# Kernel optimization log

Hardware: AMD Instinct MI355X
Metric: run time of the kernel (lower is better)

## Reference

```python
import jax, jax.numpy as jnp
import numpy as np

B, L, D, H = 4, 2048, 1024, 16
HD = D // H

def setup_inputs() -> dict:
    key = jax.random.key(0)
    k1, k2, k3, k4 = jax.random.split(key, 4)
    return {
        "Q": jax.random.normal(k1, (B, L, D), dtype=jnp.float32),
        "K": jax.random.normal(k2, (B, L, D), dtype=jnp.float32),
        "V": jax.random.normal(k3, (B, L, D), dtype=jnp.float32),
        "W_out": jax.random.normal(k4, (D, D), dtype=jnp.float32) * (1.0 / np.sqrt(D)),
        "b_out": jnp.zeros((D,), dtype=jnp.float32),
    }

def reference(Q, K, V, W_out, b_out):
    b, l, d = Q.shape
    h, hd = H, d // H
    q = Q.reshape(b, l, h, hd)
    k = K.reshape(b, l, h, hd)
    v = V.reshape(b, l, h, hd)
    # energy: [b, h, q, k]
    energy = jnp.einsum('nqhd,nkhd->nhqk', q, k)
    # NOTE: original scales by sqrt(embed_dim), not sqrt(head_dim)
    attn = jax.nn.softmax(energy / jnp.sqrt(jnp.float32(d)), axis=-1)
    out = jnp.einsum('nhql,nlhd->nqhd', attn, v).reshape(b, l, d)
    # torch nn.Linear: x @ W.T + b
    return out @ W_out.T + b_out
```

## Files before the change

### kernel.cpp

```cpp
#include <hip/hip_runtime.h>
#include <hip/hip_bf16.h>


#define B_  4
#define L_  2048
#define D_  1024
#define H_  16

typedef float  f32x4  __attribute__((ext_vector_type(4)));
typedef float  f32x16 __attribute__((ext_vector_type(16)));
typedef short  bf16x8 __attribute__((ext_vector_type(8)));
typedef short  bf16x4 __attribute__((ext_vector_type(4)));

__device__ inline unsigned short f2bf(float x) {
    union { float f; unsigned u; } v; v.f = x;
    unsigned r = v.u + 0x7FFFu + ((v.u >> 16) & 1u);
    return (unsigned short)(r >> 16);
}
__device__ inline float fast_exp2(float x) {
#if __has_builtin(__builtin_amdgcn_exp2f)
    return __builtin_amdgcn_exp2f(x);
#else
    return exp2f(x);
#endif
}
__device__ inline bf16x8 pack8s(float4 a, float4 b, float s) {
    bf16x8 r;
    r[0] = (short)f2bf(a.x * s); r[1] = (short)f2bf(a.y * s);
    r[2] = (short)f2bf(a.z * s); r[3] = (short)f2bf(a.w * s);
    r[4] = (short)f2bf(b.x * s); r[5] = (short)f2bf(b.y * s);
    r[6] = (short)f2bf(b.z * s); r[7] = (short)f2bf(b.w * s);
    return r;
}
__device__ inline unsigned cvtpk(float lo, float hi) {
    unsigned r;
    asm("v_cvt_pk_bf16_f32 %0, %1, %2" : "=v"(r) : "v"(lo), "v"(hi));
    return r;
}
#define PSWAP(a, b) asm("v_permlane32_swap_b32 %0, %1" : "+v"(a), "+v"(b))

__device__ inline f32x16 zero16() {
    f32x16 z;
    #pragma unroll
    for (int i = 0; i < 16; ++i) z[i] = 0.f;
    return z;
}
__device__ inline void gld16(const void* g, void* l) {
    __builtin_amdgcn_global_load_lds(
        (const __attribute__((address_space(1))) void*)g,
        (__attribute__((address_space(3))) void*)l, 16, 0, 0);
}

__global__ __launch_bounds__(256) void convw_kernel(const float* __restrict__ W,
                                                    unsigned short* __restrict__ Wb) {
    int i = (blockIdx.x * 256 + threadIdx.x) * 4;
    float4 v = *(const float4*)&W[i];
    bf16x4 o;
    o[0] = (short)f2bf(v.x); o[1] = (short)f2bf(v.y);
    o[2] = (short)f2bf(v.z); o[3] = (short)f2bf(v.w);
    *(bf16x4*)&Wb[i] = o;
}

__global__ __launch_bounds__(256) void convk_kernel(const float* __restrict__ K,
                                                    unsigned short* __restrict__ Kb) {
    int o = blockIdx.x * 256 + threadIdx.x;
    int d8 = o & 7; int h = (o >> 3) & 15; int key = (o >> 7) & 2047; int b = o >> 18;
    size_t base = ((size_t)(b * L_ + key) * H_ + h) * 64;
    const float* p = K + base + d8 * 8;
    float4 a = *(const float4*)p, c = *(const float4*)(p + 4);
    bf16x8 r;
    r[0] = (short)f2bf(a.x); r[1] = (short)f2bf(a.y); r[2] = (short)f2bf(a.z); r[3] = (short)f2bf(a.w);
    r[4] = (short)f2bf(c.x); r[5] = (short)f2bf(c.y); r[6] = (short)f2bf(c.z); r[7] = (short)f2bf(c.w);
    *(bf16x8*)&Kb[base + ((d8 * 8) ^ ((key & 7) * 8))] = r;
}

__global__ __launch_bounds__(256) void convv_kernel(const float* __restrict__ V,
                                                    unsigned short* __restrict__ Vb) {
    __shared__ __align__(16) unsigned short T[64 * 72];
    int tid = threadIdx.x;
    int kb_ = blockIdx.x & 31, bh = blockIdx.x >> 5;
    int b = bh >> 4, h = bh & 15, k0 = kb_ * 64;
    int kl = tid >> 4;
    int d4 = (tid & 15) * 4;
    #pragma unroll
    for (int pp = 0; pp < 4; ++pp) {
        int key = pp * 16 + kl;
        const float* p = V + ((size_t)(b * L_ + k0 + key)) * D_ + h * 64 + d4;
        float4 v = *(const float4*)p;
        T[(d4 + 0) * 72 + key] = f2bf(v.x);
        T[(d4 + 1) * 72 + key] = f2bf(v.y);
        T[(d4 + 2) * 72 + key] = f2bf(v.z);
        T[(d4 + 3) * 72 + key] = f2bf(v.w);
    }
    __syncthreads();
    #pragma unroll
    for (int i = 0; i < 2; ++i) {
        int c = i * 256 + tid; int d = c >> 3, ch = c & 7;
        bf16x8 v = *(const bf16x8*)&T[d * 72 + ch * 8];
        *(bf16x8*)&Vb[((size_t)(b * H_ + h) * 64 + d) * L_ + k0 + ((ch ^ (d & 7)) * 8)] = v;
    }
}

__global__ __launch_bounds__(256, 4) void attn_kernel(const float* __restrict__ Qg,
                                                      const unsigned short* __restrict__ Kb,
                                                      const unsigned short* __restrict__ Vb,
                                                      unsigned short* __restrict__ Og) {
    __shared__ __align__(16) unsigned short Ks[2][64 * 64];
    __shared__ __align__(16) unsigned short Vt[2][64 * 64];

    const int tid  = threadIdx.x;
    const int w    = tid >> 6;
    const int lane = tid & 63;
    const int l31  = lane & 31;
    const int hl   = lane >> 5;
    const int r7   = l31 & 7;

    const int x   = blockIdx.x;
    const int idx = x >> 3;
    const int bh  = (x & 7) * 8 + (idx & 7);
    const int qb  = idx >> 3;
    const int bz  = bh >> 4;
    const int h   = bh & 15;
    const int q0  = qb * 128;

    const float qscale = 0.04508422f;
    bf16x8 bq[4];
    {
        const int qrow = q0 + w * 32 + l31;
        const float* qp = Qg + ((size_t)(bz * L_ + qrow)) * D_ + h * 64 + hl * 8;
        #pragma unroll
        for (int dstep = 0; dstep < 4; ++dstep)
            bq[dstep] = pack8s(*(const float4*)(qp + dstep * 16),
                               *(const float4*)(qp + dstep * 16 + 4), qscale);
    }

    f32x16 o[2];
    o[0] = zero16(); o[1] = zero16();
    float lsum = 0.f;

    const unsigned short* Kbh = Kb + ((size_t)bz * L_ * H_ + h) * 64;
    const unsigned short* Vbh = Vb + (size_t)(bz * H_ + h) * 64 * L_;

    #define ISSUE(T, BUF)                                                           \
        {                                                                           \
            int k0_ = (T) * 64;                                                     \
            _Pragma("unroll")                                                       \
            for (int i = 0; i < 2; ++i) {                                           \
                int c = i * 256 + tid; int rr = c >> 3, jj = c & 7;                 \
                gld16(Kbh + (size_t)(k0_ + rr) * (H_ * 64) + jj * 8,                \
                      (char*)Ks[BUF] + (i * 256 + w * 64) * 16);                    \
                gld16(Vbh + (size_t)rr * L_ + k0_ + jj * 8,                         \
                      (char*)Vt[BUF] + (i * 256 + w * 64) * 16);                    \
            }                                                                       \
        }

    ISSUE(0, 0)

    for (int t = 0; t < 32; ++t) {
        __syncthreads();
        if (t < 31) ISSUE(t + 1, (t + 1) & 1)
        const unsigned short* ks = Ks[t & 1];
        const unsigned short* vt = Vt[t & 1];

        #pragma unroll
        for (int kk = 0; kk < 2; ++kk) {
            f32x16 s = zero16();
            #pragma unroll
            for (int dstep = 0; dstep < 4; ++dstep) {
                bf16x8 kf = *(const bf16x8*)&ks[(kk * 32 + l31) * 64 +
                                                ((((dstep << 1) | hl) ^ r7) << 3)];
                s = __builtin_amdgcn_mfma_f32_32x32x16_bf16(kf, bq[dstep], s, 0, 0, 0);
            }

            float p_[16];
            #pragma unroll
            for (int r = 0; r < 16; ++r) p_[r] = fast_exp2(s[r]);
            lsum += ((p_[0] + p_[1]) + (p_[2] + p_[3])) + ((p_[4] + p_[5]) + (p_[6] + p_[7]))
                  + ((p_[8] + p_[9]) + (p_[10] + p_[11])) + ((p_[12] + p_[13]) + (p_[14] + p_[15]));
            unsigned pk_[8];
            #pragma unroll
            for (int j = 0; j < 8; ++j) pk_[j] = cvtpk(p_[2 * j], p_[2 * j + 1]);
            PSWAP(pk_[0], pk_[2]); PSWAP(pk_[1], pk_[3]);
            PSWAP(pk_[4], pk_[6]); PSWAP(pk_[5], pk_[7]);
            union { unsigned u[4]; bf16x8 v; } a0_, a1_;
            a0_.u[0] = pk_[0]; a0_.u[1] = pk_[1]; a0_.u[2] = pk_[2]; a0_.u[3] = pk_[3];
            a1_.u[0] = pk_[4]; a1_.u[1] = pk_[5]; a1_.u[2] = pk_[6]; a1_.u[3] = pk_[7];

            #pragma unroll
            for (int kh = 0; kh < 2; ++kh) {
                const bf16x8 pf = kh ? a1_.v : a0_.v;
                const int kk2 = kk * 2 + kh;
                bf16x8 v0 = *(const bf16x8*)&vt[(l31) * 64 +
                                                ((((kk2 << 1) | hl) ^ r7) << 3)];
                bf16x8 v1 = *(const bf16x8*)&vt[(32 + l31) * 64 +
                                                ((((kk2 << 1) | hl) ^ r7) << 3)];
                o[0] = __builtin_amdgcn_mfma_f32_32x32x16_bf16(pf, v0, o[0], 0, 0, 0);
                o[1] = __builtin_amdgcn_mfma_f32_32x32x16_bf16(pf, v1, o[1], 0, 0, 0);
            }
        }
    }

    float tot = lsum + __shfl_xor(lsum, 32);
    float inv = 1.0f / tot;
    const size_t rowb0 = ((size_t)(bz * L_ + q0 + w * 32)) * D_ + h * 64;
    #pragma unroll
    for (int r = 0; r < 16; ++r) {
        const int qloc = (r & 3) + 8 * (r >> 2) + 4 * hl;
        const float invr = __shfl(inv, qloc);
        unsigned short* op = Og + rowb0 + (size_t)qloc * D_;
        op[l31]      = f2bf(o[0][r] * invr);
        op[32 + l31] = f2bf(o[1][r] * invr);
    }
}

__global__ __launch_bounds__(256, 2) void proj_kernel(const unsigned short* __restrict__ Og,
                                                      const unsigned short* __restrict__ Wb,
                                                      const float* __restrict__ bias,
                                                      float* __restrict__ Yg) {
    __shared__ unsigned short As[2][128 * 64];
    __shared__ unsigned short Bs[2][128 * 64];

    const int tid  = threadIdx.x;
    const int w    = tid >> 6;
    const int lane = tid & 63;
    const int l16  = lane & 15;
    const int quad = lane >> 4;
    const int wm   = w & 1, wn = w >> 1;

    const int m0 = blockIdx.x * 128;
    const int n0 = blockIdx.y * 128;

    f32x4 acc[4][4];
    #pragma unroll
    for (int i = 0; i < 4; ++i)
        #pragma unroll
        for (int j = 0; j < 4; ++j) acc[i][j] = (f32x4){0.f, 0.f, 0.f, 0.f};

    #define PISSUE(T, BUF)                                                          \
        {                                                                           \
            int kt_ = (T) * 64;                                                     \
            _Pragma("unroll")                                                       \
            for (int i = 0; i < 4; ++i) {                                           \
                int c = i * 256 + tid; int row = c >> 3, p = c & 7;                 \
                int j = p ^ (row & 7);                                              \
                gld16(&Og[(size_t)(m0 + row) * 1024 + kt_ + j * 8],                 \
                      (char*)As[BUF] + (i * 256 + w * 64) * 16);                    \
                gld16(&Wb[(size_t)(n0 + row) * 1024 + kt_ + j * 8],                 \
                      (char*)Bs[BUF] + (i * 256 + w * 64) * 16);                    \
            }                                                                       \
        }

    PISSUE(0, 0)

    for (int t = 0; t < 16; ++t) {
        __syncthreads();
        if (t < 15) PISSUE(t + 1, (t + 1) & 1)
        const unsigned short* as = As[t & 1];
        const unsigned short* bs = Bs[t & 1];

        #pragma unroll
        for (int ksq = 0; ksq < 2; ++ksq) {
            bf16x8 a[4], b[4];
            #pragma unroll
            for (int mt = 0; mt < 4; ++mt) {
                int row = wm * 64 + mt * 16 + l16;
                a[mt] = *(const bf16x8*)&as[row * 64 + (((ksq * 4 + quad) ^ (l16 & 7)) * 8)];
            }
            #pragma unroll
            for (int nt = 0; nt < 4; ++nt) {
                int row = wn * 64 + nt * 16 + l16;
                b[nt] = *(const bf16x8*)&bs[row * 64 + (((ksq * 4 + quad) ^ (l16 & 7)) * 8)];
            }
            #pragma unroll
            for (int mt = 0; mt < 4; ++mt)
                #pragma unroll
                for (int nt = 0; nt < 4; ++nt)
                    acc[mt][nt] = __builtin_amdgcn_mfma_f32_16x16x32_bf16(a[mt], b[nt], acc[mt][nt], 0, 0, 0);
        }
    }

    #pragma unroll
    for (int mt = 0; mt < 4; ++mt)
        #pragma unroll
        for (int nt = 0; nt < 4; ++nt) {
            int e = n0 + wn * 64 + nt * 16 + l16;
            float bv = bias[e];
            #pragma unroll
            for (int r = 0; r < 4; ++r) {
                int m = m0 + wm * 64 + mt * 16 + quad * 4 + r;
                Yg[(size_t)m * 1024 + e] = acc[mt][nt][r] + bv;
            }
        }
}

extern "C" void kernel_launch(void* const* d_in, const int* in_sizes, int n_in,
                              void* d_out, int out_size, void* d_ws, size_t ws_size,
                              hipStream_t stream) {
    const float* Q    = (const float*)d_in[0];
    const float* K    = (const float*)d_in[1];
    const float* V    = (const float*)d_in[2];
    const float* W    = (const float*)d_in[3];
    const float* bias = (const float*)d_in[4];
    float* Y = (float*)d_out;

    unsigned short* Og = (unsigned short*)d_ws;
    unsigned short* Wb = (unsigned short*)((char*)d_ws + (size_t)16 * 1024 * 1024);
    unsigned short* Kb = (unsigned short*)d_out;
    unsigned short* Vb = Kb + (size_t)B_ * H_ * L_ * 64;

    convw_kernel<<<D_ * D_ / (256 * 4), 256, 0, stream>>>(W, Wb);
    convk_kernel<<<B_ * L_ * H_ * 8 / 256, 256, 0, stream>>>(K, Kb);
    convv_kernel<<<B_ * H_ * (L_ / 64), 256, 0, stream>>>(V, Vb);
    attn_kernel<<<B_ * H_ * (L_ / 128), 256, 0, stream>>>(Q, Kb, Vb, Og);
    dim3 pg(B_ * L_ / 128, D_ / 128);
    proj_kernel<<<pg, 256, 0, stream>>>(Og, Wb, bias, Y);
}
```

Baseline: 237.6 us.

## Use 128-key tiles, MFMA row sums, and setprio in attention loop

The attention kernel now processes 128 keys per pipeline stage instead of 64. This halves the number of barrier and prefetch iterations, and it doubles the shared memory per block, so launch bounds drop from 4 to 2 blocks per CU. The softmax denominator is now computed with an extra MFMA against a vector of ones, replacing the scalar adds and the final cross-lane shuffle. That adds two MFMAs per subtile and sums the bf16-rounded probabilities, which slightly changes the numerics. s_setprio hints are also wrapped around the MFMA sections to favour matrix issue.

```diff
diff --git a/kernel.cpp b/kernel.cpp
--- a/kernel.cpp
+++ b/kernel.cpp
@@ -101,12 +101,12 @@
     }
 }
 
-__global__ __launch_bounds__(256, 4) void attn_kernel(const float* __restrict__ Qg,
+__global__ __launch_bounds__(256, 2) void attn_kernel(const float* __restrict__ Qg,
                                                       const unsigned short* __restrict__ Kb,
                                                       const unsigned short* __restrict__ Vb,
                                                       unsigned short* __restrict__ Og) {
-    __shared__ __align__(16) unsigned short Ks[2][64 * 64];
-    __shared__ __align__(16) unsigned short Vt[2][64 * 64];
+    __shared__ __align__(16) unsigned short Ks[2][128 * 64];
+    __shared__ __align__(16) unsigned short Vt[2][64 * 128];
 
     const int tid  = threadIdx.x;
     const int w    = tid >> 6;
@@ -134,49 +134,55 @@
                                *(const float4*)(qp + dstep * 16 + 4), qscale);
     }
 
+    bf16x8 ones;
+    #pragma unroll
+    for (int j = 0; j < 8; ++j) ones[j] = (short)0x3F80;
+
     f32x16 o[2];
     o[0] = zero16(); o[1] = zero16();
-    float lsum = 0.f;
+    f32x16 sums = zero16();
 
     const unsigned short* Kbh = Kb + ((size_t)bz * L_ * H_ + h) * 64;
     const unsigned short* Vbh = Vb + (size_t)(bz * H_ + h) * 64 * L_;
 
     #define ISSUE(T, BUF)                                                           \
         {                                                                           \
-            int k0_ = (T) * 64;                                                     \
+            int k0_ = (T) * 128;                                                    \
             _Pragma("unroll")                                                       \
-            for (int i = 0; i < 2; ++i) {                                           \
-                int c = i * 256 + tid; int rr = c >> 3, jj = c & 7;                 \
-                gld16(Kbh + (size_t)(k0_ + rr) * (H_ * 64) + jj * 8,                \
+            for (int i = 0; i < 4; ++i) {                                           \
+                int c = i * 256 + tid;                                              \
+                int rk = c >> 3, jk = c & 7;                                        \
+                gld16(Kbh + (size_t)(k0_ + rk) * (H_ * 64) + jk * 8,                \
                       (char*)Ks[BUF] + (i * 256 + w * 64) * 16);                    \
-                gld16(Vbh + (size_t)rr * L_ + k0_ + jj * 8,                         \
+                int rv = c >> 4, jv = c & 15;                                       \
+                gld16(Vbh + (size_t)rv * L_ + k0_ + jv * 8,                         \
                       (char*)Vt[BUF] + (i * 256 + w * 64) * 16);                    \
             }                                                                       \
         }
 
     ISSUE(0, 0)
 
-    for (int t = 0; t < 32; ++t) {
+    for (int t = 0; t < 16; ++t) {
         __syncthreads();
-        if (t < 31) ISSUE(t + 1, (t + 1) & 1)
+        if (t < 15) ISSUE(t + 1, (t + 1) & 1)
         const unsigned short* ks = Ks[t & 1];
         const unsigned short* vt = Vt[t & 1];
 
         #pragma unroll
-        for (int kk = 0; kk < 2; ++kk) {
+        for (int kk = 0; kk < 4; ++kk) {
             f32x16 s = zero16();
+            __builtin_amdgcn_s_setprio(1);
             #pragma unroll
             for (int dstep = 0; dstep < 4; ++dstep) {
                 bf16x8 kf = *(const bf16x8*)&ks[(kk * 32 + l31) * 64 +
                                                 ((((dstep << 1) | hl) ^ r7) << 3)];
                 s = __builtin_amdgcn_mfma_f32_32x32x16_bf16(kf, bq[dstep], s, 0, 0, 0);
             }
+            __builtin_amdgcn_s_setprio(0);
 
             float p_[16];
             #pragma unroll
             for (int r = 0; r < 16; ++r) p_[r] = fast_exp2(s[r]);
-            lsum += ((p_[0] + p_[1]) + (p_[2] + p_[3])) + ((p_[4] + p_[5]) + (p_[6] + p_[7]))
-                  + ((p_[8] + p_[9]) + (p_[10] + p_[11])) + ((p_[12] + p_[13]) + (p_[14] + p_[15]));
             unsigned pk_[8];
             #pragma unroll
             for (int j = 0; j < 8; ++j) pk_[j] = cvtpk(p_[2 * j], p_[2 * j + 1]);
@@ -186,27 +192,28 @@
             a0_.u[0] = pk_[0]; a0_.u[1] = pk_[1]; a0_.u[2] = pk_[2]; a0_.u[3] = pk_[3];
             a1_.u[0] = pk_[4]; a1_.u[1] = pk_[5]; a1_.u[2] = pk_[6]; a1_.u[3] = pk_[7];
 
+            __builtin_amdgcn_s_setprio(1);
+            sums = __builtin_amdgcn_mfma_f32_32x32x16_bf16(a0_.v, ones, sums, 0, 0, 0);
+            sums = __builtin_amdgcn_mfma_f32_32x32x16_bf16(a1_.v, ones, sums, 0, 0, 0);
             #pragma unroll
             for (int kh = 0; kh < 2; ++kh) {
                 const bf16x8 pf = kh ? a1_.v : a0_.v;
-                const int kk2 = kk * 2 + kh;
-                bf16x8 v0 = *(const bf16x8*)&vt[(l31) * 64 +
-                                                ((((kk2 << 1) | hl) ^ r7) << 3)];
-                bf16x8 v1 = *(const bf16x8*)&vt[(32 + l31) * 64 +
-                                                ((((kk2 << 1) | hl) ^ r7) << 3)];
+                const int oi   = (kk * 2 + kh) * 2 + hl;
+                const int slot = (oi & 8) | ((oi & 7) ^ r7);
+                bf16x8 v0 = *(const bf16x8*)&vt[(l31)      * 128 + slot * 8];
+                bf16x8 v1 = *(const bf16x8*)&vt[(32 + l31) * 128 + slot * 8];
                 o[0] = __builtin_amdgcn_mfma_f32_32x32x16_bf16(pf, v0, o[0], 0, 0, 0);
                 o[1] = __builtin_amdgcn_mfma_f32_32x32x16_bf16(pf, v1, o[1], 0, 0, 0);
             }
-        }
-    }
-
-    float tot = lsum + __shfl_xor(lsum, 32);
-    float inv = 1.0f / tot;
+            __builtin_amdgcn_s_setprio(0);
+        }
+    }
+
     const size_t rowb0 = ((size_t)(bz * L_ + q0 + w * 32)) * D_ + h * 64;
     #pragma unroll
     for (int r = 0; r < 16; ++r) {
         const int qloc = (r & 3) + 8 * (r >> 2) + 4 * hl;
-        const float invr = __shfl(inv, qloc);
+        const float invr = 1.0f / sums[r];
         unsigned short* op = Og + rowb0 + (size_t)qloc * D_;
         op[l31]      = f2bf(o[0][r] * invr);
         op[32 + l31] = f2bf(o[1][r] * invr);
```

Result: no change. 239.0 us (+0.6%).
